# Performance work log

Measured on AMD Instinct MI355X. Metric: run time of the kernel, lower is better.

The kernel has to match this reference:

```python
import jax, jax.numpy as jnp
import numpy as np

B, Hc, Wc, C, NH, SR, WS = 4, 64, 64, 256, 8, 2, 4
N = Hc * Wc


def _window_partition(x, ws, H, W):
    # x: (B, h, N, d) -> (B*h*nWin, ws*ws, d)
    Bb, h, _, d = x.shape
    x = x.reshape(Bb * h, H // ws, ws, W // ws, ws, d)
    x = x.transpose(0, 1, 3, 2, 4, 5)
    return x.reshape(-1, ws * ws, d)


def _window_reverse(win, ws, H, W, head):
    nwin = (H // ws) * (W // ws)
    Bh = win.shape[0] // nwin
    x = win.reshape(Bh, H // ws, W // ws, ws, ws, -1).transpose(0, 1, 3, 2, 4, 5).reshape(Bh, H, W, -1)
    Bb = Bh // head
    x = x.reshape(Bb, head, H, W, -1).transpose(0, 2, 3, 1, 4)  # heads interleave into channels
    return x.reshape(Bb, H * W, -1)


def _layernorm(x, w, b):
    m = x.mean(-1, keepdims=True)
    v = x.var(-1, keepdims=True)
    return (x - m) / jnp.sqrt(v + 1e-5) * w + b


def setup_inputs() -> dict:
    key = jax.random.key(0)
    ks = jax.random.split(key, 16)
    lin = lambda k, i, o: 0.02 * jax.random.normal(k, (i, o), jnp.float32)
    inp = {
        'x': jax.random.normal(ks[0], (B, N, C), jnp.float32),
        'q1_w': lin(ks[1], C, C // 2), 'q1_b': jnp.zeros((C // 2,), jnp.float32),
        'kv1_w': lin(ks[2], C, C), 'kv1_b': jnp.zeros((C,), jnp.float32),
        'q2_w': lin(ks[3], C, C // 2), 'q2_b': jnp.zeros((C // 2,), jnp.float32),
        'kv2_w': lin(ks[4], C, C), 'kv2_b': jnp.zeros((C,), jnp.float32),
        'lepe_w': lin(ks[5], C, C), 'lepe_b': jnp.zeros((C,), jnp.float32),
        'lepe_conv_w': jnp.sqrt(2.0 / 9.0) * jax.random.normal(ks[6], (C, 1, 3, 3), jnp.float32),
        'lepe_conv_b': jnp.zeros((C,), jnp.float32),
        'sr_w': jnp.sqrt(2.0 / (SR * SR * C)) * jax.random.normal(ks[7], (C, C, SR, SR), jnp.float32),
        'sr_b': jnp.zeros((C,), jnp.float32),
        'norm_w': jnp.ones((C,), jnp.float32), 'norm_b': jnp.zeros((C,), jnp.float32),
        'proj_w': lin(ks[8], C, C), 'proj_b': jnp.zeros((C,), jnp.float32),
        'H': Hc, 'W': Wc,
    }
    return inp


def reference(x, q1_w, q1_b, kv1_w, kv1_b, q2_w, q2_b, kv2_w, kv2_b,
              lepe_w, lepe_b, lepe_conv_w, lepe_conv_b, sr_w, sr_b,
              norm_w, norm_b, proj_w, proj_b, H, W):
    Bb, Nn, Cc = x.shape
    h2 = NH // 2
    d = Cc // NH
    sr = sr_w.shape[-1]
    scale = d ** -0.5
    ws = WS

    # lepe: linear -> depthwise 3x3 conv
    l = (x @ lepe_w + lepe_b).transpose(0, 2, 1).reshape(Bb, Cc, H, W)
    l = jax.lax.conv_general_dilated(l, lepe_conv_w, (1, 1), ((1, 1), (1, 1)),
                                     dimension_numbers=('NCHW', 'OIHW', 'NCHW'),
                                     feature_group_count=Cc) + lepe_conv_b[None, :, None, None]
    lepe = l.reshape(Bb, Cc, Nn).transpose(0, 2, 1)

    # branch 1: spatial-reduction global attention
    q1 = (x @ q1_w + q1_b).reshape(Bb, Nn, h2, d).transpose(0, 2, 1, 3)
    x_img = x.transpose(0, 2, 1).reshape(Bb, Cc, H, W)
    xs = jax.lax.conv_general_dilated(x_img, sr_w, (sr, sr), 'VALID',
                                      dimension_numbers=('NCHW', 'OIHW', 'NCHW')) + sr_b[None, :, None, None]
    N1 = (H // sr) * (W // sr)
    xs = xs.reshape(Bb, Cc, N1).transpose(0, 2, 1)
    xs = jax.nn.gelu(_layernorm(xs, norm_w, norm_b), approximate=False)
    kv1 = (xs @ kv1_w + kv1_b).reshape(Bb, N1, 2, h2, d).transpose(2, 0, 3, 1, 4)
    k1, v1 = kv1[0], kv1[1]
    attn1 = jax.nn.softmax(jnp.einsum('bhnd,bhmd->bhnm', q1, k1) * scale, axis=-1)
    x1 = jnp.einsum('bhnm,bhmd->bnhd', attn1, v1).reshape(Bb, Nn, Cc // 2)
    g = jax.lax.stop_gradient(attn1).mean(1).mean(1).reshape(Bb, H // sr, W // sr)
    g = jnp.repeat(jnp.repeat(g, sr, axis=1), sr, axis=2)  # nearest upsample to (B,H,W)

    # branch 2: Swin-style windowed attention (window 4)
    q2 = (x @ q2_w + q2_b).reshape(Bb, Nn, h2, d).transpose(0, 2, 1, 3)
    kv2 = (x @ kv2_w + kv2_b).reshape(Bb, Nn, 2, h2, d).transpose(2, 0, 3, 1, 4)
    k2, v2 = kv2[0], kv2[1]
    q2w = _window_partition(q2, ws, H, W)
    k2w = _window_partition(k2, ws, H, W)
    v2w = _window_partition(v2, ws, H, W)
    attn2 = jax.nn.softmax(jnp.einsum('wnd,wmd->wnm', q2w, k2w) * scale, axis=-1)
    x2 = jnp.einsum('wnm,wmd->wnd', attn2, v2w)
    x2 = _window_reverse(x2, ws, H, W, h2)
    nwin = (H // ws) * (W // ws)
    lm = jax.lax.stop_gradient(attn2).reshape(Bb, h2, nwin, ws * ws, ws * ws).mean(1).mean(2)
    lm = lm.reshape(Bb, H // ws, W // ws, ws, ws).transpose(0, 1, 3, 2, 4).reshape(Bb, H, W)

    out = jnp.concatenate([x1, x2], axis=-1)
    p = (out + lepe) @ proj_w + proj_b
    out = p + p  # proj_drop is identity at p=0.0, so x = drop(p) + p = 2p

    mask = lm + g
    mask1 = mask.reshape(Bb, H * W)
    mask2 = mask.transpose(0, 2, 1).reshape(Bb, H * W)
    return out, mask1, mask2
```

## Files before the change

### kernel.cpp

```cpp
#include <hip/hip_runtime.h>
#include <hip/hip_bf16.h>
#include <math.h>

typedef __hip_bfloat16 bf16;
typedef __attribute__((ext_vector_type(8))) short bf16x8;
typedef __attribute__((ext_vector_type(4))) short bf16x4;
typedef __attribute__((ext_vector_type(4))) float f32x4;

__device__ __forceinline__ float b2f(bf16 v) { return __bfloat162float(v); }
__device__ __forceinline__ bf16  f2b(float v) { return __float2bfloat16(v); }
__device__ __forceinline__ float s2f(short v) { return __uint_as_float(((unsigned)(unsigned short)v) << 16); }

__global__ void detect_dtype(const void* x, int* flag)
{
    __shared__ int cnt;
    if (threadIdx.x == 0) cnt = 0;
    __syncthreads();
    const unsigned* w = (const unsigned*)x;
    int sane = 0;
    for (int i = threadIdx.x; i < 2048; i += 256) {
        unsigned lo = (w[i] & 0xFFFFu) << 16;
        float v = __uint_as_float(lo);
        float a = fabsf(v);
        if (v == 0.f || (a > 1e-8f && a < 1e4f)) sane++;
    }
    atomicAdd(&cnt, sane);
    __syncthreads();
    if (threadIdx.x == 0) *flag = (cnt < 1640) ? 1 : 0;
}

__global__ void convert_x4(const void* __restrict__ src, bf16* __restrict__ dst,
                           const int* __restrict__ flag)
{
    int i = blockIdx.x * 256 + threadIdx.x;
    bf16 tmp[4];
    if (*flag) {
        float4 v = ((const float4*)src)[i];
        tmp[0] = f2b(v.x); tmp[1] = f2b(v.y); tmp[2] = f2b(v.z); tmp[3] = f2b(v.w);
        *(bf16x4*)&dst[i * 4] = *(bf16x4*)tmp;
    } else {
        ((bf16x4*)dst)[i] = ((const bf16x4*)src)[i];
    }
}

struct MiscArgs {
    const void* srw;  bf16* srwT;
    const void* dww;  bf16* dwT;
    const void* psrc[10]; bf16* pdst[10]; int pn[10];
};
__global__ void convert_misc(MiscArgs a, const int* __restrict__ flag)
{
    int blk = blockIdx.x, t = threadIdx.x;
    int fl = *flag;
    if (blk < 1024) {
        int o = blk * 256 + t;
        int co = o >> 10, kg = o & 1023;
        int e = kg >> 8, ci = kg & 255;
        int si = co * 1024 + ci * 4 + e;
        float v = fl ? ((const float*)a.srw)[si] : s2f(((const short*)a.srw)[si]);
        a.srwT[o] = f2b(v);
    } else if (blk < 1033) {
        int o = (blk - 1024) * 256 + t;
        if (o >= 2304) return;
        int k = o >> 8, c = o & 255;
        float v = fl ? ((const float*)a.dww)[c * 9 + k] : s2f(((const short*)a.dww)[c * 9 + k]);
        a.dwT[o] = f2b(v);
    } else {
        int bi = blk - 1033;
        int n = a.pn[bi];
        const void* s = a.psrc[bi];
        bf16* d = a.pdst[bi];
        for (int i = t; i < n; i += 256)
            d[i] = fl ? f2b(((const float*)s)[i]) : f2b(s2f(((const short*)s)[i]));
    }
}

struct WTArgs { const void* src[6]; bf16* dst[6]; int N[6]; int blkoff[7]; };
__global__ void convert_wT_multi(WTArgs a, const int* __restrict__ flag)
{
    int blk = blockIdx.x;
    int ti = 0;
    while (blk >= a.blkoff[ti + 1]) ++ti;
    int o = (blk - a.blkoff[ti]) * 256 + threadIdx.x;
    int n = o >> 8, k = o & 255;
    int N = a.N[ti];
    float v = (*flag) ? ((const float*)a.src[ti])[k * N + n]
                      : s2f(((const short*)a.src[ti])[k * N + n]);
    a.dst[ti][o] = f2b(v);
}

__global__ __launch_bounds__(256) void gemm_qkv128(
    const bf16* __restrict__ A, const bf16* __restrict__ WT, const bf16* __restrict__ bias,
    bf16* __restrict__ Cl, bf16* __restrict__ Cq1, bf16* __restrict__ Cq2, bf16* __restrict__ Ckv2)
{
    __shared__ bf16 As[128][40];
    __shared__ bf16 Bs[128][40];
    int t = threadIdx.x;
    int m0 = blockIdx.x * 128, ybase = blockIdx.y * 128;
    int w = t >> 6, l = t & 63, lane16 = l & 15, quad = l >> 4;
    int wr = w >> 1, wc = w & 1;
    int sr = t >> 1, sc = (t & 1) * 16;
    f32x4 acc[4][4] = {};
    for (int k0 = 0; k0 < 256; k0 += 32) {
        *(bf16x8*)&As[sr][sc]     = *(const bf16x8*)&A[(size_t)(m0 + sr) * 256 + k0 + sc];
        *(bf16x8*)&As[sr][sc + 8] = *(const bf16x8*)&A[(size_t)(m0 + sr) * 256 + k0 + sc + 8];
        *(bf16x8*)&Bs[sr][sc]     = *(const bf16x8*)&WT[(size_t)(ybase + sr) * 256 + k0 + sc];
        *(bf16x8*)&Bs[sr][sc + 8] = *(const bf16x8*)&WT[(size_t)(ybase + sr) * 256 + k0 + sc + 8];
        __syncthreads();
        bf16x8 a[4], b[4];
        #pragma unroll
        for (int i = 0; i < 4; ++i) {
            a[i] = *(const bf16x8*)&As[wr * 64 + i * 16 + lane16][quad * 8];
            b[i] = *(const bf16x8*)&Bs[wc * 64 + i * 16 + lane16][quad * 8];
        }
        #pragma unroll
        for (int i = 0; i < 4; ++i)
            #pragma unroll
            for (int j = 0; j < 4; ++j)
                acc[i][j] = __builtin_amdgcn_mfma_f32_16x16x32_bf16(a[i], b[j], acc[i][j], 0, 0, 0);
        __syncthreads();
    }
    bf16* C; int N, cbase;
    if (ybase < 256)      { C = Cl;   N = 256; cbase = ybase; }
    else if (ybase < 384) { C = Cq1;  N = 128; cbase = ybase - 256; }
    else if (ybase < 512) { C = Cq2;  N = 128; cbase = ybase - 384; }
    else                  { C = Ckv2; N = 256; cbase = ybase - 512; }
    #pragma unroll
    for (int j = 0; j < 4; ++j) {
        int gcol = ybase + wc * 64 + j * 16 + lane16;
        float bv = b2f(bias[gcol]);
        int col = cbase + wc * 64 + j * 16 + lane16;
        #pragma unroll
        for (int i = 0; i < 4; ++i)
            #pragma unroll
            for (int r = 0; r < 4; ++r) {
                int row = m0 + wr * 64 + i * 16 + quad * 4 + r;
                C[(size_t)row * N + col] = f2b(acc[i][j][r] + bv);
            }
    }
}

__global__ __launch_bounds__(256) void gemm_proj128(
    const bf16* __restrict__ A, const bf16* __restrict__ A2,
    const bf16* __restrict__ WT, const bf16* __restrict__ bias,
    void* __restrict__ dout, const int* __restrict__ flag)
{
    __shared__ bf16 As[128][40];
    __shared__ bf16 Bs[128][40];
    int t = threadIdx.x;
    int m0 = blockIdx.x * 128, n0 = blockIdx.y * 128;
    int w = t >> 6, l = t & 63, lane16 = l & 15, quad = l >> 4;
    int wr = w >> 1, wc = w & 1;
    int sr = t >> 1, sc = (t & 1) * 16;
    f32x4 acc[4][4] = {};
    for (int k0 = 0; k0 < 256; k0 += 32) {
        #pragma unroll
        for (int hh = 0; hh < 2; ++hh) {
            bf16x8 va = *(const bf16x8*)&A[(size_t)(m0 + sr) * 256 + k0 + sc + hh * 8];
            bf16x8 vb = *(const bf16x8*)&A2[(size_t)(m0 + sr) * 256 + k0 + sc + hh * 8];
            bf16 tmp[8];
            #pragma unroll
            for (int q = 0; q < 8; ++q) tmp[q] = f2b(s2f(va[q]) + s2f(vb[q]));
            *(bf16x8*)&As[sr][sc + hh * 8] = *(bf16x8*)tmp;
        }
        *(bf16x8*)&Bs[sr][sc]     = *(const bf16x8*)&WT[(size_t)(n0 + sr) * 256 + k0 + sc];
        *(bf16x8*)&Bs[sr][sc + 8] = *(const bf16x8*)&WT[(size_t)(n0 + sr) * 256 + k0 + sc + 8];
        __syncthreads();
        bf16x8 a[4], b[4];
        #pragma unroll
        for (int i = 0; i < 4; ++i) {
            a[i] = *(const bf16x8*)&As[wr * 64 + i * 16 + lane16][quad * 8];
            b[i] = *(const bf16x8*)&Bs[wc * 64 + i * 16 + lane16][quad * 8];
        }
        #pragma unroll
        for (int i = 0; i < 4; ++i)
            #pragma unroll
            for (int j = 0; j < 4; ++j)
                acc[i][j] = __builtin_amdgcn_mfma_f32_16x16x32_bf16(a[i], b[j], acc[i][j], 0, 0, 0);
        __syncthreads();
    }
    #pragma unroll
    for (int j = 0; j < 4; ++j) {
        int col = n0 + wc * 64 + j * 16 + lane16;
        float bv = b2f(bias[col]);
        #pragma unroll
        for (int i = 0; i < 4; ++i)
            #pragma unroll
            for (int r = 0; r < 4; ++r) {
                int row = m0 + wr * 64 + i * 16 + quad * 4 + r;
                float rv = (acc[i][j][r] + bv) * 2.f;
                size_t o = (size_t)row * 256 + col;
                if (*flag) ((float*)dout)[o] = rv;
                else       ((bf16*)dout)[o] = f2b(rv);
            }
    }
}

__global__ __launch_bounds__(256) void gemm_sr_mfma(
    const bf16* __restrict__ x, const bf16* __restrict__ WT,
    const bf16* __restrict__ bias, bf16* __restrict__ C)
{
    __shared__ bf16 As[64][40];
    __shared__ bf16 Bs[64][40];
    int t = threadIdx.x;
    int m0 = blockIdx.x * 64, n0 = blockIdx.y * 64;
    int w = t >> 6, l = t & 63, lane16 = l & 15, quad = l >> 4;
    int sr = t >> 2, sc = (t & 3) * 8;
    int brow = m0 + sr;
    int b = brow >> 10, p = brow & 1023;
    int pi = p >> 5, pj = p & 31;
    f32x4 acc[4] = {};
    for (int k0 = 0; k0 < 1024; k0 += 32) {
        int kg = k0 + sc;
        int e = kg >> 8, ci = kg & 255;
        int di = e >> 1, dj = e & 1;
        int n = (2 * pi + di) * 64 + 2 * pj + dj;
        *(bf16x8*)&As[sr][sc] = *(const bf16x8*)&x[(size_t)((b << 12) + n) * 256 + ci];
        *(bf16x8*)&Bs[sr][sc] = *(const bf16x8*)&WT[(size_t)(n0 + sr) * 1024 + kg];
        __syncthreads();
        bf16x8 a = *(const bf16x8*)&As[w * 16 + lane16][quad * 8];
        #pragma unroll
        for (int ct = 0; ct < 4; ++ct) {
            bf16x8 bb = *(const bf16x8*)&Bs[ct * 16 + lane16][quad * 8];
            acc[ct] = __builtin_amdgcn_mfma_f32_16x16x32_bf16(a, bb, acc[ct], 0, 0, 0);
        }
        __syncthreads();
    }
    #pragma unroll
    for (int ct = 0; ct < 4; ++ct) {
        int col = n0 + ct * 16 + lane16;
        float bv = b2f(bias[col]);
        #pragma unroll
        for (int r = 0; r < 4; ++r) {
            int row = m0 + w * 16 + quad * 4 + r;
            C[(size_t)row * 256 + col] = f2b(acc[ct][r] + bv);
        }
    }
}

__global__ __launch_bounds__(256) void gemm_kv1(
    const bf16* __restrict__ A, const bf16* __restrict__ WT, const bf16* __restrict__ bias,
    bf16* __restrict__ k1, bf16* __restrict__ v1T)
{
    __shared__ bf16 As[64][40];
    __shared__ bf16 Bs[64][40];
    int t = threadIdx.x;
    int m0 = blockIdx.x * 64, n0 = blockIdx.y * 64;
    int w = t >> 6, l = t & 63, lane16 = l & 15, quad = l >> 4;
    int sr = t >> 2, sc = (t & 3) * 8;
    f32x4 acc[4] = {};
    for (int k0 = 0; k0 < 256; k0 += 32) {
        *(bf16x8*)&As[sr][sc] = *(const bf16x8*)&A[(size_t)(m0 + sr) * 256 + k0 + sc];
        *(bf16x8*)&Bs[sr][sc] = *(const bf16x8*)&WT[(size_t)(n0 + sr) * 256 + k0 + sc];
        __syncthreads();
        bf16x8 a = *(const bf16x8*)&As[w * 16 + lane16][quad * 8];
        #pragma unroll
        for (int ct = 0; ct < 4; ++ct) {
            bf16x8 b = *(const bf16x8*)&Bs[ct * 16 + lane16][quad * 8];
            acc[ct] = __builtin_amdgcn_mfma_f32_16x16x32_bf16(a, b, acc[ct], 0, 0, 0);
        }
        __syncthreads();
    }
    #pragma unroll
    for (int ct = 0; ct < 4; ++ct) {
        int col = n0 + ct * 16 + lane16;
        float bv = b2f(bias[col]);
        #pragma unroll
        for (int r = 0; r < 4; ++r) {
            int row = m0 + w * 16 + quad * 4 + r;
            float val = acc[ct][r] + bv;
            int bb = row >> 10, key = row & 1023;
            if (col < 128) {
                k1[(size_t)row * 128 + col] = f2b(val);
            } else {
                int h = (col - 128) >> 5, ch = (col - 128) & 31;
                v1T[(size_t)((bb * 4 + h) * 32 + ch) * 1024 + key] = f2b(val);
            }
        }
    }
}

__global__ __launch_bounds__(256) void dwconv3p(
    const bf16* __restrict__ lin, const bf16* __restrict__ dwT,
    const bf16* __restrict__ bias, bf16* __restrict__ out)
{
    int tid = blockIdx.x * 256 + threadIdx.x;
    int c0 = (tid & 31) * 8;
    int j  = (tid >> 5) & 63;
    int i  = ((tid >> 11) & 31) * 2;
    int b  = tid >> 16;
    float acc0[8], acc1[8];
    bf16x8 bv = *(const bf16x8*)&bias[c0];
    #pragma unroll
    for (int q = 0; q < 8; ++q) { acc0[q] = s2f(bv[q]); acc1[q] = s2f(bv[q]); }
    bf16x8 wv[3][3];
    #pragma unroll
    for (int di = 0; di < 3; ++di)
        #pragma unroll
        for (int dj = 0; dj < 3; ++dj)
            wv[di][dj] = *(const bf16x8*)&dwT[(di * 3 + dj) * 256 + c0];
    #pragma unroll
    for (int r = -1; r <= 2; ++r) {
        int ii = i + r;
        if (ii < 0 || ii > 63) continue;
        #pragma unroll
        for (int dj = 0; dj < 3; ++dj) {
            int jj = j + dj - 1;
            if (jj < 0 || jj > 63) continue;
            bf16x8 xv = *(const bf16x8*)&lin[(size_t)((b << 12) + ii * 64 + jj) * 256 + c0];
            if (r <= 1) {
                bf16x8 w0 = wv[r + 1][dj];
                #pragma unroll
                for (int q = 0; q < 8; ++q) acc0[q] += s2f(xv[q]) * s2f(w0[q]);
            }
            if (r >= 0) {
                bf16x8 w1 = wv[r][dj];
                #pragma unroll
                for (int q = 0; q < 8; ++q) acc1[q] += s2f(xv[q]) * s2f(w1[q]);
            }
        }
    }
    bf16 ov[8];
    #pragma unroll
    for (int q = 0; q < 8; ++q) ov[q] = f2b(acc0[q]);
    *(bf16x8*)&out[(size_t)((b << 12) + i * 64 + j) * 256 + c0] = *(bf16x8*)ov;
    #pragma unroll
    for (int q = 0; q < 8; ++q) ov[q] = f2b(acc1[q]);
    *(bf16x8*)&out[(size_t)((b << 12) + (i + 1) * 64 + j) * 256 + c0] = *(bf16x8*)ov;
}

__global__ __launch_bounds__(256) void ln_gelu_w(
    const bf16* __restrict__ xin, const bf16* __restrict__ nw,
    const bf16* __restrict__ nb, bf16* __restrict__ xout)
{
    int w = threadIdx.x >> 6, lane = threadIdx.x & 63;
    int r = blockIdx.x * 4 + w;
    bf16x4 xv = *(const bf16x4*)&xin[(size_t)r * 256 + lane * 4];
    float v[4];
    #pragma unroll
    for (int j = 0; j < 4; ++j) v[j] = s2f(xv[j]);
    float s = v[0] + v[1] + v[2] + v[3];
    #pragma unroll
    for (int o = 1; o <= 32; o <<= 1) s += __shfl_xor(s, o);
    float mean = s * (1.f / 256.f);
    float ss = 0.f;
    #pragma unroll
    for (int j = 0; j < 4; ++j) { float d = v[j] - mean; ss += d * d; }
    #pragma unroll
    for (int o = 1; o <= 32; o <<= 1) ss += __shfl_xor(ss, o);
    float inv = rsqrtf(ss * (1.f / 256.f) + 1e-5f);
    bf16x4 wv = *(const bf16x4*)&nw[lane * 4];
    bf16x4 bv = *(const bf16x4*)&nb[lane * 4];
    bf16 ov[4];
    #pragma unroll
    for (int j = 0; j < 4; ++j) {
        float y = (v[j] - mean) * inv * s2f(wv[j]) + s2f(bv[j]);
        ov[j] = f2b(0.5f * y * (1.f + erff(y * 0.70710678118654752f)));
    }
    *(bf16x4*)&xout[(size_t)r * 256 + lane * 4] = *(bf16x4*)ov;
}

__global__ __launch_bounds__(512) void attn1_split(
    const bf16* __restrict__ q1, const bf16* __restrict__ k1,
    const bf16* __restrict__ v1T, bf16* __restrict__ attn_out, float* __restrict__ g)
{
    __shared__ bf16 PTT[8][16][72];
    __shared__ float gp[1024];
    __shared__ float Lcmb[4][16];
    __shared__ float rls[4][16];
    __shared__ __align__(16) float Ocmb[4][16][36];

    int t = threadIdx.x;
    int blk = blockIdx.x;
    int qc = blk & 63, h = (blk >> 6) & 3, b = blk >> 8;
    int n0 = qc * 64;
    int w = t >> 6, l = t & 63, lane16 = l & 15, quad = l >> 4;
    int grp = w >> 2, qg = w & 3;
    const float scale = 0.17677669529663687f;

    const bf16* Kbase = k1 + (size_t)b * 1024 * 128 + 32 * h + (size_t)(grp * 512) * 128;
    const bf16* Vbase = v1T + (size_t)((b * 4 + h) * 32) * 1024 + grp * 512;
    bf16x8 qa = *(const bf16x8*)&q1[(size_t)(b * 4096 + n0 + 16 * qg + lane16) * 128 + 32 * h + quad * 8];

    for (int i = t; i < 1024; i += 512) gp[i] = 0.f;

    bf16* ptt = &PTT[w][0][0];

    const bf16* Krow  = Kbase + (size_t)lane16 * 128 + quad * 8;
    const bf16* Vrow0 = Vbase + (size_t)lane16 * 1024;
    const bf16* Vrow1 = Vbase + (size_t)(16 + lane16) * 1024;

    float lacc = 0.f;
    f32x4 oT0 = {}, oT1 = {};

    for (int ktl = 0; ktl < 8; ++ktl) {
        bf16x8 kf[4];
        #pragma unroll
        for (int st = 0; st < 4; ++st)
            kf[st] = *(const bf16x8*)&Krow[(size_t)(ktl * 64 + st * 16) * 128];
        #pragma unroll
        for (int st = 0; st < 4; ++st) {
            f32x4 z = {0.f, 0.f, 0.f, 0.f};
            f32x4 sT = __builtin_amdgcn_mfma_f32_16x16x32_bf16(kf[st], qa, z, 0, 0, 0);
            bf16 pk[4];
            #pragma unroll
            for (int r = 0; r < 4; ++r) {
                float p = __expf(sT[r] * scale);
                lacc += p;
                pk[r] = f2b(p);
            }
            *(bf16x4*)&ptt[lane16 * 72 + st * 16 + quad * 4] = *(bf16x4*)pk;
        }
        #pragma unroll
        for (int kh = 0; kh < 2; ++kh) {
            bf16x8 vf0 = *(const bf16x8*)&Vrow0[ktl * 64 + kh * 32 + quad * 8];
            bf16x8 vf1 = *(const bf16x8*)&Vrow1[ktl * 64 + kh * 32 + quad * 8];
            bf16x8 pf  = *(const bf16x8*)&ptt[lane16 * 72 + kh * 32 + quad * 8];
            oT0 = __builtin_amdgcn_mfma_f32_16x16x32_bf16(vf0, pf, oT0, 0, 0, 0);
            oT1 = __builtin_amdgcn_mfma_f32_16x16x32_bf16(vf1, pf, oT1, 0, 0, 0);
        }
    }

    lacc += __shfl_xor(lacc, 16);
    lacc += __shfl_xor(lacc, 32);

    if (grp == 1) {
        if (quad == 0) Lcmb[qg][lane16] = lacc;
        *(f32x4*)&Ocmb[qg][lane16][quad * 4]      = oT0;
        *(f32x4*)&Ocmb[qg][lane16][16 + quad * 4] = oT1;
    }
    __syncthreads();
    if (grp == 0) {
        float ltot = lacc + Lcmb[qg][lane16];
        float rl = 1.f / ltot;
        if (quad == 0) rls[qg][lane16] = rl;
        f32x4 p0 = *(const f32x4*)&Ocmb[qg][lane16][quad * 4];
        f32x4 p1 = *(const f32x4*)&Ocmb[qg][lane16][16 + quad * 4];
        bf16 ov0[4], ov1[4];
        #pragma unroll
        for (int r = 0; r < 4; ++r) {
            ov0[r] = f2b((oT0[r] + p0[r]) * rl);
            ov1[r] = f2b((oT1[r] + p1[r]) * rl);
        }
        size_t ro = (size_t)(b * 4096 + n0 + 16 * qg + lane16) * 256 + 32 * h;
        *(bf16x4*)&attn_out[ro + quad * 4]      = *(bf16x4*)ov0;
        *(bf16x4*)&attn_out[ro + 16 + quad * 4] = *(bf16x4*)ov1;
    }
    __syncthreads();

    float rlq[4];
    #pragma unroll
    for (int r = 0; r < 4; ++r) rlq[r] = rls[qg][quad * 4 + r];

    for (int ktl = 0; ktl < 8; ++ktl) {
        #pragma unroll
        for (int st = 0; st < 4; ++st) {
            bf16x8 kf = *(const bf16x8*)&Kbase[(size_t)(ktl * 64 + st * 16 + lane16) * 128 + quad * 8];
            f32x4 z = {0.f, 0.f, 0.f, 0.f};
            f32x4 s = __builtin_amdgcn_mfma_f32_16x16x32_bf16(qa, kf, z, 0, 0, 0);
            float cs = 0.f;
            #pragma unroll
            for (int r = 0; r < 4; ++r) cs += __expf(s[r] * scale) * rlq[r];
            cs += __shfl_xor(cs, 16);
            cs += __shfl_xor(cs, 32);
            if (quad == 0) atomicAdd(&gp[grp * 512 + ktl * 64 + st * 16 + lane16], cs);
        }
    }
    __syncthreads();

    for (int i = t; i < 1024; i += 512)
        atomicAdd(&g[(b << 10) + i], gp[i] * (1.f / 16384.f));
}

__global__ __launch_bounds__(256) void attn2_mfma(
    const bf16* __restrict__ q2, const bf16* __restrict__ kv2,
    bf16* __restrict__ attn_out, float* __restrict__ lm)
{
    __shared__ bf16 PT2[4][16 * 40];
    __shared__ float lmw[16];
    int t = threadIdx.x;
    int blk = blockIdx.x;
    int b = blk >> 8, win = blk & 255;
    int wi = win >> 4, wj = win & 15;
    int h = t >> 6, l = t & 63, lane16 = l & 15, quad = l >> 4;
    const float scale = 0.17677669529663687f;

    if (t < 16) lmw[t] = 0.f;
    bf16* ptt = &PT2[h][0];
    {
        bf16 zz[4] = {};
        *(bf16x4*)&ptt[lane16 * 40 + 16 + quad * 4] = *(bf16x4*)zz;
    }
    __syncthreads();

    size_t base = (size_t)(b * 4096);
    int r0 = wi * 4, c0w = wj * 4;
    int tq = (r0 + (lane16 >> 2)) * 64 + c0w + (lane16 & 3);

    bf16x8 qa = *(const bf16x8*)&q2[(base + tq) * 128 + h * 32 + quad * 8];
    bf16x8 kf = *(const bf16x8*)&kv2[(base + tq) * 256 + h * 32 + quad * 8];

    f32x4 z = {0.f, 0.f, 0.f, 0.f};
    f32x4 sT = __builtin_amdgcn_mfma_f32_16x16x32_bf16(kf, qa, z, 0, 0, 0);
    float sv[4];
    #pragma unroll
    for (int r = 0; r < 4; ++r) sv[r] = sT[r] * scale;
    float mx = fmaxf(fmaxf(sv[0], sv[1]), fmaxf(sv[2], sv[3]));
    mx = fmaxf(mx, __shfl_xor(mx, 16));
    mx = fmaxf(mx, __shfl_xor(mx, 32));
    float p[4], lsum = 0.f;
    #pragma unroll
    for (int r = 0; r < 4; ++r) { p[r] = __expf(sv[r] - mx); lsum += p[r]; }
    lsum += __shfl_xor(lsum, 16);
    lsum += __shfl_xor(lsum, 32);
    float rl = 1.f / lsum;
    bf16 pk[4];
    #pragma unroll
    for (int r = 0; r < 4; ++r) { p[r] *= rl; pk[r] = f2b(p[r]); }
    *(bf16x4*)&ptt[lane16 * 40 + quad * 4] = *(bf16x4*)pk;

    bf16x8 vf0 = {}, vf1 = {};
    if (quad < 2) {
        #pragma unroll
        for (int jj = 0; jj < 8; ++jj) {
            int key = quad * 8 + jj;
            int tk = (r0 + (key >> 2)) * 64 + c0w + (key & 3);
            const short* vp = (const short*)&kv2[(base + tk) * 256 + 128 + h * 32];
            vf0[jj] = vp[lane16];
            vf1[jj] = vp[16 + lane16];
        }
    }
    bf16x8 pf = *(const bf16x8*)&ptt[lane16 * 40 + quad * 8];
    f32x4 o0 = __builtin_amdgcn_mfma_f32_16x16x32_bf16(vf0, pf, z, 0, 0, 0);
    f32x4 o1 = __builtin_amdgcn_mfma_f32_16x16x32_bf16(vf1, pf, z, 0, 0, 0);
    {
        bf16 ov0[4], ov1[4];
        #pragma unroll
        for (int r = 0; r < 4; ++r) { ov0[r] = f2b(o0[r]); ov1[r] = f2b(o1[r]); }
        bf16* op = attn_out + (base + tq) * 256 + 128 + h * 32;
        *(bf16x4*)&op[quad * 4]      = *(bf16x4*)ov0;
        *(bf16x4*)&op[16 + quad * 4] = *(bf16x4*)ov1;
    }

    #pragma unroll
    for (int r = 0; r < 4; ++r) {
        float c = p[r];
        c += __shfl_xor(c, 1);
        c += __shfl_xor(c, 2);
        c += __shfl_xor(c, 4);
        c += __shfl_xor(c, 8);
        if (lane16 == 0) atomicAdd(&lmw[quad * 4 + r], c);
    }
    __syncthreads();
    if (t < 16) {
        int nk = (r0 + (t >> 2)) * 64 + c0w + (t & 3);
        lm[(b << 12) + nk] = lmw[t] * (1.f / 64.f);
    }
}

__global__ void mask_combine(const float* __restrict__ lm, const float* __restrict__ g,
                             void* __restrict__ dout, const int* __restrict__ flag)
{
    int tid = blockIdx.x * 256 + threadIdx.x;
    int b = tid >> 12, n = tid & 4095;
    int i = n >> 6, j = n & 63;
    float v = lm[tid] + g[(b << 10) + (i >> 1) * 32 + (j >> 1)];
    size_t o1 = (size_t)4194304 + (b << 12) + i * 64 + j;
    size_t o2 = (size_t)4194304 + 16384 + (b << 12) + j * 64 + i;
    if (*flag) { ((float*)dout)[o1] = v; ((float*)dout)[o2] = v; }
    else       { ((bf16*)dout)[o1] = f2b(v); ((bf16*)dout)[o2] = f2b(v); }
}

extern "C" void kernel_launch(void* const* d_in, const int* in_sizes, int n_in,
                              void* d_out, int out_size, void* d_ws, size_t ws_size,
                              hipStream_t stream)
{
    char* ws = (char*)d_ws;
    size_t off = 0;
    auto alloc = [&](size_t bytes) {
        void* p = ws + off;
        off += (bytes + 255) & ~(size_t)255;
        return p;
    };
    bf16* cx       = (bf16*)alloc((size_t)4194304 * 2);
    bf16* lepe_lin = (bf16*)alloc((size_t)4194304 * 2);
    bf16* attn_out = lepe_lin;
    bf16* lepe     = (bf16*)alloc((size_t)4194304 * 2);
    bf16* q1buf    = (bf16*)alloc((size_t)2097152 * 2);
    bf16* q2buf    = (bf16*)alloc((size_t)2097152 * 2);
    bf16* kv2buf   = (bf16*)alloc((size_t)4194304 * 2);
    bf16* xs_pre   = (bf16*)alloc((size_t)1048576 * 2);
    bf16* k1buf    = xs_pre;
    bf16* v1Tbuf   = xs_pre + 524288;
    bf16* xs       = (bf16*)alloc((size_t)1048576 * 2);
    bf16* wTqkv    = (bf16*)alloc((size_t)196608 * 2);
    bf16* kv1_wT   = (bf16*)alloc(65536 * 2);
    bf16* proj_wT  = (bf16*)alloc(65536 * 2);
    bf16* sr_wT    = (bf16*)alloc(262144 * 2);
    bf16* dwT      = (bf16*)alloc(2304 * 2);
    bf16* bcat     = (bf16*)alloc(768 * 2);
    bf16* ckv1b    = (bf16*)alloc(256 * 2);
    bf16* csrb     = (bf16*)alloc(256 * 2);
    bf16* cnw      = (bf16*)alloc(256 * 2);
    bf16* cnb      = (bf16*)alloc(256 * 2);
    bf16* cpb      = (bf16*)alloc(256 * 2);
    bf16* clcb     = (bf16*)alloc(256 * 2);
    float* gbuf    = (float*)alloc(4096 * 4);
    float* lmbuf   = (float*)alloc(16384 * 4);
    int*   flag    = (int*)alloc(256);

    detect_dtype<<<1, 256, 0, stream>>>(d_in[0], flag);

    convert_x4<<<4096, 256, 0, stream>>>(d_in[0], cx, flag);

    MiscArgs ma;
    ma.srw = d_in[13]; ma.srwT = sr_wT;
    ma.dww = d_in[11]; ma.dwT = dwT;
    ma.psrc[0] = d_in[10]; ma.pdst[0] = bcat;       ma.pn[0] = 256;
    ma.psrc[1] = d_in[2];  ma.pdst[1] = bcat + 256; ma.pn[1] = 128;
    ma.psrc[2] = d_in[6];  ma.pdst[2] = bcat + 384; ma.pn[2] = 128;
    ma.psrc[3] = d_in[8];  ma.pdst[3] = bcat + 512; ma.pn[3] = 256;
    ma.psrc[4] = d_in[4];  ma.pdst[4] = ckv1b;      ma.pn[4] = 256;
    ma.psrc[5] = d_in[14]; ma.pdst[5] = csrb;       ma.pn[5] = 256;
    ma.psrc[6] = d_in[15]; ma.pdst[6] = cnw;        ma.pn[6] = 256;
    ma.psrc[7] = d_in[16]; ma.pdst[7] = cnb;        ma.pn[7] = 256;
    ma.psrc[8] = d_in[18]; ma.pdst[8] = cpb;        ma.pn[8] = 256;
    ma.psrc[9] = d_in[12]; ma.pdst[9] = clcb;       ma.pn[9] = 256;
    convert_misc<<<1043, 256, 0, stream>>>(ma, flag);

    WTArgs wa;
    wa.src[0] = d_in[9];  wa.dst[0] = wTqkv;             wa.N[0] = 256;
    wa.src[1] = d_in[1];  wa.dst[1] = wTqkv + 256 * 256; wa.N[1] = 128;
    wa.src[2] = d_in[5];  wa.dst[2] = wTqkv + 384 * 256; wa.N[2] = 128;
    wa.src[3] = d_in[7];  wa.dst[3] = wTqkv + 512 * 256; wa.N[3] = 256;
    wa.src[4] = d_in[3];  wa.dst[4] = kv1_wT;            wa.N[4] = 256;
    wa.src[5] = d_in[17]; wa.dst[5] = proj_wT;           wa.N[5] = 256;
    int bo[7] = {0, 256, 384, 512, 768, 1024, 1280};
    for (int i = 0; i < 7; ++i) wa.blkoff[i] = bo[i];
    convert_wT_multi<<<1280, 256, 0, stream>>>(wa, flag);

    hipMemsetAsync(gbuf, 0, 4096 * 4, stream);

    gemm_qkv128<<<dim3(128, 6), 256, 0, stream>>>(cx, wTqkv, bcat, lepe_lin, q1buf, q2buf, kv2buf);
    gemm_sr_mfma<<<dim3(64, 4), 256, 0, stream>>>(cx, sr_wT, csrb, xs_pre);
    ln_gelu_w<<<1024, 256, 0, stream>>>(xs_pre, cnw, cnb, xs);
    gemm_kv1<<<dim3(64, 4), 256, 0, stream>>>(xs, kv1_wT, ckv1b, k1buf, v1Tbuf);
    dwconv3p<<<1024, 256, 0, stream>>>(lepe_lin, dwT, clcb, lepe);
    attn1_split<<<1024, 512, 0, stream>>>(q1buf, k1buf, v1Tbuf, attn_out, gbuf);
    attn2_mfma<<<1024, 256, 0, stream>>>(q2buf, kv2buf, attn_out, lmbuf);
    gemm_proj128<<<dim3(128, 2), 256, 0, stream>>>(attn_out, lepe, proj_wT, cpb, d_out, flag);
    mask_combine<<<64, 256, 0, stream>>>(lmbuf, gbuf, d_out, flag);
}
```

Before: 289.8 us.

## Merge conversion kernels, fold mask combine into proj, restage attn1 K/V in LDS

Folds the three input/weight conversion kernels and the gbuf memset into one convert_all launch. It also runs the mask-combine work as extra blocks of the projection GEMM grid, so two launches go away. Separately, attn1 drops its two-group key split with a cross-group combine and uses 256 threads that loop over all keys. K and V tiles are now double-buffered through LDS with register prefetch. This cuts launch overhead and the combine synchronization, but halves the threads per block and adds a barrier every key tile.

```diff
diff --git a/kernel.cpp b/kernel.cpp
--- a/kernel.cpp
+++ b/kernel.cpp
@@ -29,64 +29,61 @@
     if (threadIdx.x == 0) *flag = (cnt < 1640) ? 1 : 0;
 }
 
-__global__ void convert_x4(const void* __restrict__ src, bf16* __restrict__ dst,
-                           const int* __restrict__ flag)
-{
-    int i = blockIdx.x * 256 + threadIdx.x;
-    bf16 tmp[4];
-    if (*flag) {
-        float4 v = ((const float4*)src)[i];
-        tmp[0] = f2b(v.x); tmp[1] = f2b(v.y); tmp[2] = f2b(v.z); tmp[3] = f2b(v.w);
-        *(bf16x4*)&dst[i * 4] = *(bf16x4*)tmp;
-    } else {
-        ((bf16x4*)dst)[i] = ((const bf16x4*)src)[i];
-    }
-}
-
-struct MiscArgs {
+struct AllArgs {
+    const void* x; bf16* cx;
     const void* srw;  bf16* srwT;
     const void* dww;  bf16* dwT;
     const void* psrc[10]; bf16* pdst[10]; int pn[10];
+    const void* wsrc[6]; bf16* wdst[6]; int wN[6]; int wblkoff[7];
+    float* gbuf;
 };
-__global__ void convert_misc(MiscArgs a, const int* __restrict__ flag)
+__global__ void convert_all(AllArgs a, const int* __restrict__ flag)
 {
     int blk = blockIdx.x, t = threadIdx.x;
     int fl = *flag;
-    if (blk < 1024) {
-        int o = blk * 256 + t;
+    if (blk < 4096) {
+        int i = blk * 256 + t;
+        if (fl) {
+            float4 v = ((const float4*)a.x)[i];
+            bf16 tmp[4];
+            tmp[0] = f2b(v.x); tmp[1] = f2b(v.y); tmp[2] = f2b(v.z); tmp[3] = f2b(v.w);
+            *(bf16x4*)&a.cx[i * 4] = *(bf16x4*)tmp;
+        } else {
+            ((bf16x4*)a.cx)[i] = ((const bf16x4*)a.x)[i];
+        }
+    } else if (blk < 5120) {
+        int o = (blk - 4096) * 256 + t;
         int co = o >> 10, kg = o & 1023;
         int e = kg >> 8, ci = kg & 255;
         int si = co * 1024 + ci * 4 + e;
         float v = fl ? ((const float*)a.srw)[si] : s2f(((const short*)a.srw)[si]);
         a.srwT[o] = f2b(v);
-    } else if (blk < 1033) {
-        int o = (blk - 1024) * 256 + t;
+    } else if (blk < 5129) {
+        int o = (blk - 5120) * 256 + t;
         if (o >= 2304) return;
         int k = o >> 8, c = o & 255;
         float v = fl ? ((const float*)a.dww)[c * 9 + k] : s2f(((const short*)a.dww)[c * 9 + k]);
         a.dwT[o] = f2b(v);
-    } else {
-        int bi = blk - 1033;
+    } else if (blk < 5139) {
+        int bi = blk - 5129;
         int n = a.pn[bi];
         const void* s = a.psrc[bi];
         bf16* d = a.pdst[bi];
         for (int i = t; i < n; i += 256)
             d[i] = fl ? f2b(((const float*)s)[i]) : f2b(s2f(((const short*)s)[i]));
-    }
-}
-
-struct WTArgs { const void* src[6]; bf16* dst[6]; int N[6]; int blkoff[7]; };
-__global__ void convert_wT_multi(WTArgs a, const int* __restrict__ flag)
-{
-    int blk = blockIdx.x;
-    int ti = 0;
-    while (blk >= a.blkoff[ti + 1]) ++ti;
-    int o = (blk - a.blkoff[ti]) * 256 + threadIdx.x;
-    int n = o >> 8, k = o & 255;
-    int N = a.N[ti];
-    float v = (*flag) ? ((const float*)a.src[ti])[k * N + n]
-                      : s2f(((const short*)a.src[ti])[k * N + n]);
-    a.dst[ti][o] = f2b(v);
+    } else if (blk < 6419) {
+        int wblk = blk - 5139;
+        int ti = 0;
+        while (wblk >= a.wblkoff[ti + 1]) ++ti;
+        int o = (wblk - a.wblkoff[ti]) * 256 + t;
+        int n = o >> 8, k = o & 255;
+        int N = a.wN[ti];
+        float v = fl ? ((const float*)a.wsrc[ti])[k * N + n]
+                     : s2f(((const short*)a.wsrc[ti])[k * N + n]);
+        a.wdst[ti][o] = f2b(v);
+    } else {
+        for (int i = t; i < 4096; i += 256) a.gbuf[i] = 0.f;
+    }
 }
 
 __global__ __launch_bounds__(256) void gemm_qkv128(
@@ -143,8 +140,21 @@
 __global__ __launch_bounds__(256) void gemm_proj128(
     const bf16* __restrict__ A, const bf16* __restrict__ A2,
     const bf16* __restrict__ WT, const bf16* __restrict__ bias,
+    const float* __restrict__ lm, const float* __restrict__ g,
     void* __restrict__ dout, const int* __restrict__ flag)
 {
+    if (blockIdx.y == 2) {
+        if (blockIdx.x >= 64) return;
+        int tid = blockIdx.x * 256 + threadIdx.x;
+        int b = tid >> 12, n = tid & 4095;
+        int i = n >> 6, j = n & 63;
+        float v = lm[tid] + g[(b << 10) + (i >> 1) * 32 + (j >> 1)];
+        size_t o1 = (size_t)4194304 + (b << 12) + i * 64 + j;
+        size_t o2 = (size_t)4194304 + 16384 + (b << 12) + j * 64 + i;
+        if (*flag) { ((float*)dout)[o1] = v; ((float*)dout)[o2] = v; }
+        else       { ((bf16*)dout)[o1] = f2b(v); ((bf16*)dout)[o2] = f2b(v); }
+        return;
+    }
     __shared__ bf16 As[128][40];
     __shared__ bf16 Bs[128][40];
     int t = threadIdx.x;
@@ -360,44 +370,50 @@
     *(bf16x4*)&xout[(size_t)r * 256 + lane * 4] = *(bf16x4*)ov;
 }
 
-__global__ __launch_bounds__(512) void attn1_split(
+__global__ __launch_bounds__(256) void attn1_split(
     const bf16* __restrict__ q1, const bf16* __restrict__ k1,
     const bf16* __restrict__ v1T, bf16* __restrict__ attn_out, float* __restrict__ g)
 {
-    __shared__ bf16 PTT[8][16][72];
+    __shared__ bf16 Kt[2][64][40];
+    __shared__ bf16 Vt[2][32][68];
+    __shared__ bf16 PTT[4][16][72];
     __shared__ float gp[1024];
-    __shared__ float Lcmb[4][16];
-    __shared__ float rls[4][16];
-    __shared__ __align__(16) float Ocmb[4][16][36];
 
     int t = threadIdx.x;
     int blk = blockIdx.x;
     int qc = blk & 63, h = (blk >> 6) & 3, b = blk >> 8;
     int n0 = qc * 64;
     int w = t >> 6, l = t & 63, lane16 = l & 15, quad = l >> 4;
-    int grp = w >> 2, qg = w & 3;
     const float scale = 0.17677669529663687f;
 
-    const bf16* Kbase = k1 + (size_t)b * 1024 * 128 + 32 * h + (size_t)(grp * 512) * 128;
-    const bf16* Vbase = v1T + (size_t)((b * 4 + h) * 32) * 1024 + grp * 512;
-    bf16x8 qa = *(const bf16x8*)&q1[(size_t)(b * 4096 + n0 + 16 * qg + lane16) * 128 + 32 * h + quad * 8];
-
-    for (int i = t; i < 1024; i += 512) gp[i] = 0.f;
-
+    const bf16* Kbase = k1 + (size_t)b * 1024 * 128 + 32 * h;
+    const bf16* Vbase = v1T + (size_t)((b * 4 + h) * 32) * 1024;
+    bf16x8 qa = *(const bf16x8*)&q1[(size_t)(b * 4096 + n0 + 16 * w + lane16) * 128 + 32 * h + quad * 8];
+
+    for (int i = t; i < 1024; i += 256) gp[i] = 0.f;
+
+    int sr = t >> 2, sc = (t & 3) * 8;
+    int vrow = t >> 3, vcol = (t & 7) * 8;
     bf16* ptt = &PTT[w][0][0];
 
-    const bf16* Krow  = Kbase + (size_t)lane16 * 128 + quad * 8;
-    const bf16* Vrow0 = Vbase + (size_t)lane16 * 1024;
-    const bf16* Vrow1 = Vbase + (size_t)(16 + lane16) * 1024;
+    *(bf16x8*)&Kt[0][sr][sc]     = *(const bf16x8*)&Kbase[(size_t)sr * 128 + sc];
+    *(bf16x8*)&Vt[0][vrow][vcol] = *(const bf16x8*)&Vbase[(size_t)vrow * 1024 + vcol];
+    __syncthreads();
 
     float lacc = 0.f;
     f32x4 oT0 = {}, oT1 = {};
 
-    for (int ktl = 0; ktl < 8; ++ktl) {
+    for (int ktl = 0; ktl < 16; ++ktl) {
+        int cur = ktl & 1;
+        bf16x8 knext, vnext;
+        if (ktl < 15) {
+            knext = *(const bf16x8*)&Kbase[(size_t)((ktl + 1) * 64 + sr) * 128 + sc];
+            vnext = *(const bf16x8*)&Vbase[(size_t)vrow * 1024 + (ktl + 1) * 64 + vcol];
+        }
         bf16x8 kf[4];
         #pragma unroll
         for (int st = 0; st < 4; ++st)
-            kf[st] = *(const bf16x8*)&Krow[(size_t)(ktl * 64 + st * 16) * 128];
+            kf[st] = *(const bf16x8*)&Kt[cur][st * 16 + lane16][quad * 8];
         #pragma unroll
         for (int st = 0; st < 4; ++st) {
             f32x4 z = {0.f, 0.f, 0.f, 0.f};
@@ -413,46 +429,39 @@
         }
         #pragma unroll
         for (int kh = 0; kh < 2; ++kh) {
-            bf16x8 vf0 = *(const bf16x8*)&Vrow0[ktl * 64 + kh * 32 + quad * 8];
-            bf16x8 vf1 = *(const bf16x8*)&Vrow1[ktl * 64 + kh * 32 + quad * 8];
             bf16x8 pf  = *(const bf16x8*)&ptt[lane16 * 72 + kh * 32 + quad * 8];
+            bf16x8 vf0 = *(const bf16x8*)&Vt[cur][lane16][kh * 32 + quad * 8];
+            bf16x8 vf1 = *(const bf16x8*)&Vt[cur][16 + lane16][kh * 32 + quad * 8];
             oT0 = __builtin_amdgcn_mfma_f32_16x16x32_bf16(vf0, pf, oT0, 0, 0, 0);
             oT1 = __builtin_amdgcn_mfma_f32_16x16x32_bf16(vf1, pf, oT1, 0, 0, 0);
         }
+        if (ktl < 15) {
+            *(bf16x8*)&Kt[cur ^ 1][sr][sc]     = knext;
+            *(bf16x8*)&Vt[cur ^ 1][vrow][vcol] = vnext;
+        }
+        __syncthreads();
     }
 
     lacc += __shfl_xor(lacc, 16);
     lacc += __shfl_xor(lacc, 32);
-
-    if (grp == 1) {
-        if (quad == 0) Lcmb[qg][lane16] = lacc;
-        *(f32x4*)&Ocmb[qg][lane16][quad * 4]      = oT0;
-        *(f32x4*)&Ocmb[qg][lane16][16 + quad * 4] = oT1;
-    }
-    __syncthreads();
-    if (grp == 0) {
-        float ltot = lacc + Lcmb[qg][lane16];
-        float rl = 1.f / ltot;
-        if (quad == 0) rls[qg][lane16] = rl;
-        f32x4 p0 = *(const f32x4*)&Ocmb[qg][lane16][quad * 4];
-        f32x4 p1 = *(const f32x4*)&Ocmb[qg][lane16][16 + quad * 4];
+    float rl = 1.f / lacc;
+    {
         bf16 ov0[4], ov1[4];
         #pragma unroll
         for (int r = 0; r < 4; ++r) {
-            ov0[r] = f2b((oT0[r] + p0[r]) * rl);
-            ov1[r] = f2b((oT1[r] + p1[r]) * rl);
-        }
-        size_t ro = (size_t)(b * 4096 + n0 + 16 * qg + lane16) * 256 + 32 * h;
+            ov0[r] = f2b(oT0[r] * rl);
+            ov1[r] = f2b(oT1[r] * rl);
+        }
+        size_t ro = (size_t)(b * 4096 + n0 + 16 * w + lane16) * 256 + 32 * h;
         *(bf16x4*)&attn_out[ro + quad * 4]      = *(bf16x4*)ov0;
         *(bf16x4*)&attn_out[ro + 16 + quad * 4] = *(bf16x4*)ov1;
     }
-    __syncthreads();
 
     float rlq[4];
     #pragma unroll
-    for (int r = 0; r < 4; ++r) rlq[r] = rls[qg][quad * 4 + r];
-
-    for (int ktl = 0; ktl < 8; ++ktl) {
+    for (int r = 0; r < 4; ++r) rlq[r] = __shfl(rl, quad * 4 + r);
+
+    for (int ktl = 0; ktl < 16; ++ktl) {
         #pragma unroll
         for (int st = 0; st < 4; ++st) {
             bf16x8 kf = *(const bf16x8*)&Kbase[(size_t)(ktl * 64 + st * 16 + lane16) * 128 + quad * 8];
@@ -463,12 +472,12 @@
             for (int r = 0; r < 4; ++r) cs += __expf(s[r] * scale) * rlq[r];
             cs += __shfl_xor(cs, 16);
             cs += __shfl_xor(cs, 32);
-            if (quad == 0) atomicAdd(&gp[grp * 512 + ktl * 64 + st * 16 + lane16], cs);
+            if (quad == 0) atomicAdd(&gp[ktl * 64 + st * 16 + lane16], cs);
         }
     }
     __syncthreads();
 
-    for (int i = t; i < 1024; i += 512)
+    for (int i = t; i < 1024; i += 256)
         atomicAdd(&g[(b << 10) + i], gp[i] * (1.f / 16384.f));
 }
 
@@ -556,19 +565,6 @@
         int nk = (r0 + (t >> 2)) * 64 + c0w + (t & 3);
         lm[(b << 12) + nk] = lmw[t] * (1.f / 64.f);
     }
-}
-
-__global__ void mask_combine(const float* __restrict__ lm, const float* __restrict__ g,
-                             void* __restrict__ dout, const int* __restrict__ flag)
-{
-    int tid = blockIdx.x * 256 + threadIdx.x;
-    int b = tid >> 12, n = tid & 4095;
-    int i = n >> 6, j = n & 63;
-    float v = lm[tid] + g[(b << 10) + (i >> 1) * 32 + (j >> 1)];
-    size_t o1 = (size_t)4194304 + (b << 12) + i * 64 + j;
-    size_t o2 = (size_t)4194304 + 16384 + (b << 12) + j * 64 + i;
-    if (*flag) { ((float*)dout)[o1] = v; ((float*)dout)[o2] = v; }
-    else       { ((bf16*)dout)[o1] = f2b(v); ((bf16*)dout)[o2] = f2b(v); }
 }
 
 extern "C" void kernel_launch(void* const* d_in, const int* in_sizes, int n_in,
@@ -611,43 +607,38 @@
 
     detect_dtype<<<1, 256, 0, stream>>>(d_in[0], flag);
 
-    convert_x4<<<4096, 256, 0, stream>>>(d_in[0], cx, flag);
-
-    MiscArgs ma;
-    ma.srw = d_in[13]; ma.srwT = sr_wT;
-    ma.dww = d_in[11]; ma.dwT = dwT;
-    ma.psrc[0] = d_in[10]; ma.pdst[0] = bcat;       ma.pn[0] = 256;
-    ma.psrc[1] = d_in[2];  ma.pdst[1] = bcat + 256; ma.pn[1] = 128;
-    ma.psrc[2] = d_in[6];  ma.pdst[2] = bcat + 384; ma.pn[2] = 128;
-    ma.psrc[3] = d_in[8];  ma.pdst[3] = bcat + 512; ma.pn[3] = 256;
-    ma.psrc[4] = d_in[4];  ma.pdst[4] = ckv1b;      ma.pn[4] = 256;
-    ma.psrc[5] = d_in[14]; ma.pdst[5] = csrb;       ma.pn[5] = 256;
-    ma.psrc[6] = d_in[15]; ma.pdst[6] = cnw;        ma.pn[6] = 256;
-    ma.psrc[7] = d_in[16]; ma.pdst[7] = cnb;        ma.pn[7] = 256;
-    ma.psrc[8] = d_in[18]; ma.pdst[8] = cpb;        ma.pn[8] = 256;
-    ma.psrc[9] = d_in[12]; ma.pdst[9] = clcb;       ma.pn[9] = 256;
-    convert_misc<<<1043, 256, 0, stream>>>(ma, flag);
-
-    WTArgs wa;
-    wa.src[0] = d_in[9];  wa.dst[0] = wTqkv;             wa.N[0] = 256;
-    wa.src[1] = d_in[1];  wa.dst[1] = wTqkv + 256 * 256; wa.N[1] = 128;
-    wa.src[2] = d_in[5];  wa.dst[2] = wTqkv + 384 * 256; wa.N[2] = 128;
-    wa.src[3] = d_in[7];  wa.dst[3] = wTqkv + 512 * 256; wa.N[3] = 256;
-    wa.src[4] = d_in[3];  wa.dst[4] = kv1_wT;            wa.N[4] = 256;
-    wa.src[5] = d_in[17]; wa.dst[5] = proj_wT;           wa.N[5] = 256;
+    AllArgs aa;
+    aa.x = d_in[0]; aa.cx = cx;
+    aa.srw = d_in[13]; aa.srwT = sr_wT;
+    aa.dww = d_in[11]; aa.dwT = dwT;
+    aa.psrc[0] = d_in[10]; aa.pdst[0] = bcat;       aa.pn[0] = 256;
+    aa.psrc[1] = d_in[2];  aa.pdst[1] = bcat + 256; aa.pn[1] = 128;
+    aa.psrc[2] = d_in[6];  aa.pdst[2] = bcat + 384; aa.pn[2] = 128;
+    aa.psrc[3] = d_in[8];  aa.pdst[3] = bcat + 512; aa.pn[3] = 256;
+    aa.psrc[4] = d_in[4];  aa.pdst[4] = ckv1b;      aa.pn[4] = 256;
+    aa.psrc[5] = d_in[14]; aa.pdst[5] = csrb;       aa.pn[5] = 256;
+    aa.psrc[6] = d_in[15]; aa.pdst[6] = cnw;        aa.pn[6] = 256;
+    aa.psrc[7] = d_in[16]; aa.pdst[7] = cnb;        aa.pn[7] = 256;
+    aa.psrc[8] = d_in[18]; aa.pdst[8] = cpb;        aa.pn[8] = 256;
+    aa.psrc[9] = d_in[12]; aa.pdst[9] = clcb;       aa.pn[9] = 256;
+    aa.wsrc[0] = d_in[9];  aa.wdst[0] = wTqkv;             aa.wN[0] = 256;
+    aa.wsrc[1] = d_in[1];  aa.wdst[1] = wTqkv + 256 * 256; aa.wN[1] = 128;
+    aa.wsrc[2] = d_in[5];  aa.wdst[2] = wTqkv + 384 * 256; aa.wN[2] = 128;
+    aa.wsrc[3] = d_in[7];  aa.wdst[3] = wTqkv + 512 * 256; aa.wN[3] = 256;
+    aa.wsrc[4] = d_in[3];  aa.wdst[4] = kv1_wT;            aa.wN[4] = 256;
+    aa.wsrc[5] = d_in[17]; aa.wdst[5] = proj_wT;           aa.wN[5] = 256;
     int bo[7] = {0, 256, 384, 512, 768, 1024, 1280};
-    for (int i = 0; i < 7; ++i) wa.blkoff[i] = bo[i];
-    convert_wT_multi<<<1280, 256, 0, stream>>>(wa, flag);
-
-    hipMemsetAsync(gbuf, 0, 4096 * 4, stream);
+    for (int i = 0; i < 7; ++i) aa.wblkoff[i] = bo[i];
+    aa.gbuf = gbuf;
+    convert_all<<<6420, 256, 0, stream>>>(aa, flag);
 
     gemm_qkv128<<<dim3(128, 6), 256, 0, stream>>>(cx, wTqkv, bcat, lepe_lin, q1buf, q2buf, kv2buf);
     gemm_sr_mfma<<<dim3(64, 4), 256, 0, stream>>>(cx, sr_wT, csrb, xs_pre);
     ln_gelu_w<<<1024, 256, 0, stream>>>(xs_pre, cnw, cnb, xs);
     gemm_kv1<<<dim3(64, 4), 256, 0, stream>>>(xs, kv1_wT, ckv1b, k1buf, v1Tbuf);
     dwconv3p<<<1024, 256, 0, stream>>>(lepe_lin, dwT, clcb, lepe);
-    attn1_split<<<1024, 512, 0, stream>>>(q1buf, k1buf, v1Tbuf, attn_out, gbuf);
+    attn1_split<<<1024, 256, 0, stream>>>(q1buf, k1buf, v1Tbuf, attn_out, gbuf);
     attn2_mfma<<<1024, 256, 0, stream>>>(q2buf, kv2buf, attn_out, lmbuf);
-    gemm_proj128<<<dim3(128, 2), 256, 0, stream>>>(attn_out, lepe, proj_wT, cpb, d_out, flag);
-    mask_combine<<<64, 256, 0, stream>>>(lmbuf, gbuf, d_out, flag);
-}
+    gemm_proj128<<<dim3(128, 3), 256, 0, stream>>>(attn_out, lepe, proj_wT, cpb,
+                                                   lmbuf, gbuf, d_out, flag);
+}
```

Result: faster. 245.4 us (-15.3%).
